# Kernel optimization log

Hardware: AMD Instinct MI355X
Metric: run time of the kernel (lower is better)

## Reference

```python
import jax, jax.numpy as jnp
import numpy as np

N_NODES = 100000
N_EDGES = 3200000
N_GRAPHS = 64
NODE_FEATS = 32
LATENT = [32, 32, 32, 1]
OUT_DIM = 128
TOTAL_LATENT = sum(LATENT)  # 97


def setup_inputs() -> dict:
    key = jax.random.key(0)
    ks = jax.random.split(key, 16)
    node_feat = jax.random.normal(ks[0], (N_NODES, NODE_FEATS), dtype=jnp.float32)
    src = jax.random.randint(ks[1], (N_EDGES,), 0, N_NODES)
    dst = jax.random.randint(ks[2], (N_EDGES,), 0, N_NODES)
    graph_ids = jnp.sort(jax.random.randint(ks[3], (N_NODES,), 0, N_GRAPHS))
    # layer weights: Linear(in, out) -> W [in, out], b [out]
    dims = [NODE_FEATS] + LATENT
    inp = {
        'node_feat': node_feat,
        'src': src,
        'dst': dst,
        'graph_ids': graph_ids,
        'num_graphs': N_GRAPHS,
    }
    for i in range(len(LATENT)):
        inp[f'W{i}'] = 0.1 * jax.random.normal(ks[4 + 2 * i], (dims[i], dims[i + 1]), dtype=jnp.float32)
        inp[f'b{i}'] = 0.1 * jax.random.normal(ks[5 + 2 * i], (dims[i + 1],), dtype=jnp.float32)
    inp['Wout'] = 0.1 * jax.random.normal(ks[12], (TOTAL_LATENT, OUT_DIM), dtype=jnp.float32)
    inp['bout'] = 0.1 * jax.random.normal(ks[13], (OUT_DIM,), dtype=jnp.float32)
    return inp


def reference(node_feat, W0, b0, W1, b1, W2, b2, W3, b3, Wout, bout,
              src, dst, graph_ids, num_graphs):
    N = node_feat.shape[0]
    # node_degs = deg + 1 (adjacency row sums + 1)
    degs = jax.ops.segment_sum(jnp.ones_like(dst, dtype=node_feat.dtype), dst, num_segments=N)
    node_degs = (degs + 1.0)[:, None]  # [N, 1]

    params = [(W0, b0), (W1, b1), (W2, b2), (W3, b3)]
    h = node_feat
    cats = []
    for W, b in params:
        # n2npool = A @ h + h  (sparse SpMM via edge-list segment sum)
        agg = jax.ops.segment_sum(h[src], dst, num_segments=N) + h
        h = jnp.tanh((agg @ W + b) / node_degs)
        cats.append(h)
    hcat = jnp.concatenate(cats, axis=1)  # [N, 97]

    # per-graph sum pooling
    pooled = jax.ops.segment_sum(hcat, graph_ids, num_segments=num_graphs)  # [G, 97]
    # relu(relu(linear)) == relu(linear)
    out = jax.nn.relu(pooled @ Wout + bout)
    return out
```

## Files before the change

kernel.cpp:

```cpp
#include <hip/hip_runtime.h>
#include <hip/hip_bf16.h>


#define NFEAT 32
#define TOTLAT 97
#define NGRAPH 64
#define OUTDIM 128
#define BSHIFT 9
#define NPB 512
#define MAXBUCK 256
#define CH 8192

__global__ __launch_bounds__(256) void hist_kernel(const int* __restrict__ dst,
                                                   int* __restrict__ bucket_cnt,
                                                   int E, int nbuck) {
    __shared__ int h[MAXBUCK];
    for (int i = threadIdx.x; i < nbuck; i += blockDim.x) h[i] = 0;
    __syncthreads();
    int e0 = blockIdx.x * CH, e1 = min(e0 + CH, E);
    const int4* d4 = (const int4*)dst;
    int k0 = e0 >> 2, nk = (e1 - e0) >> 2;
    for (int k = k0 + threadIdx.x; k < k0 + nk; k += blockDim.x) {
        int4 v = d4[k];
        atomicAdd(&h[v.x >> BSHIFT], 1);
        atomicAdd(&h[v.y >> BSHIFT], 1);
        atomicAdd(&h[v.z >> BSHIFT], 1);
        atomicAdd(&h[v.w >> BSHIFT], 1);
    }
    for (int e = e0 + (nk << 2) + threadIdx.x; e < e1; e += blockDim.x)
        atomicAdd(&h[dst[e] >> BSHIFT], 1);
    __syncthreads();
    for (int i = threadIdx.x; i < nbuck; i += blockDim.x)
        if (h[i]) atomicAdd(&bucket_cnt[i], h[i]);
}

__global__ void bucket_scan_kernel(const int* __restrict__ bucket_cnt,
                                   int* __restrict__ bucket_start,
                                   int* __restrict__ bucket_cursor,
                                   int* __restrict__ row_ptr,
                                   int N, int E, int nbuck) {
    __shared__ int s[MAXBUCK];
    int i = threadIdx.x;
    int v = (i < nbuck) ? bucket_cnt[i] : 0;
    s[i] = v;
    __syncthreads();
    for (int d = 1; d < MAXBUCK; d <<= 1) {
        int t = (i >= d) ? s[i - d] : 0;
        __syncthreads();
        if (i >= d) s[i] += t;
        __syncthreads();
    }
    if (i < nbuck) {
        int excl = s[i] - v;
        bucket_start[i] = excl;
        bucket_cursor[i] = excl;
    }
    if (i == 0) { bucket_start[nbuck] = E; row_ptr[N] = E; }
}

__global__ __launch_bounds__(256) void part_kernel(const int* __restrict__ src,
                                                   const int* __restrict__ dst,
                                                   int* __restrict__ bucket_cursor,
                                                   int2* __restrict__ pairs,
                                                   int E, int nbuck) {
    __shared__ int h[MAXBUCK];
    __shared__ int gb[MAXBUCK];
    for (int i = threadIdx.x; i < nbuck; i += blockDim.x) h[i] = 0;
    __syncthreads();
    int e0 = blockIdx.x * CH, e1 = min(e0 + CH, E);
    const int4* d4 = (const int4*)dst;
    const int4* s4 = (const int4*)src;
    int k0 = e0 >> 2, nk = (e1 - e0) >> 2;
    for (int k = k0 + threadIdx.x; k < k0 + nk; k += blockDim.x) {
        int4 v = d4[k];
        atomicAdd(&h[v.x >> BSHIFT], 1);
        atomicAdd(&h[v.y >> BSHIFT], 1);
        atomicAdd(&h[v.z >> BSHIFT], 1);
        atomicAdd(&h[v.w >> BSHIFT], 1);
    }
    for (int e = e0 + (nk << 2) + threadIdx.x; e < e1; e += blockDim.x)
        atomicAdd(&h[dst[e] >> BSHIFT], 1);
    __syncthreads();
    for (int i = threadIdx.x; i < nbuck; i += blockDim.x) {
        int c = h[i];
        gb[i] = c ? atomicAdd(&bucket_cursor[i], c) : 0;
        h[i] = 0;
    }
    __syncthreads();
    for (int k = k0 + threadIdx.x; k < k0 + nk; k += blockDim.x) {
        int4 d = d4[k];
        int4 s = s4[k];
        int b, r;
        b = d.x >> BSHIFT; r = atomicAdd(&h[b], 1); pairs[gb[b] + r] = make_int2(s.x, d.x);
        b = d.y >> BSHIFT; r = atomicAdd(&h[b], 1); pairs[gb[b] + r] = make_int2(s.y, d.y);
        b = d.z >> BSHIFT; r = atomicAdd(&h[b], 1); pairs[gb[b] + r] = make_int2(s.z, d.z);
        b = d.w >> BSHIFT; r = atomicAdd(&h[b], 1); pairs[gb[b] + r] = make_int2(s.w, d.w);
    }
    for (int e = e0 + (nk << 2) + threadIdx.x; e < e1; e += blockDim.x) {
        int dv = dst[e];
        int b = dv >> BSHIFT;
        int r = atomicAdd(&h[b], 1);
        pairs[gb[b] + r] = make_int2(src[e], dv);
    }
}

__global__ __launch_bounds__(NPB) void csr_kernel(const int2* __restrict__ pairs,
                                                  const int* __restrict__ bucket_start,
                                                  int* __restrict__ row_ptr,
                                                  int* __restrict__ col_idx,
                                                  float* __restrict__ inv_deg, int N) {
    __shared__ int deg[NPB];
    __shared__ int scn[NPB];
    int b = blockIdx.x;
    int n0 = b << BSHIFT;
    int tid = threadIdx.x;
    deg[tid] = 0;
    __syncthreads();
    int e0 = bucket_start[b], e1 = bucket_start[b + 1];
    for (int e = e0 + tid; e < e1; e += NPB) {
        int2 p = pairs[e];
        atomicAdd(&deg[p.y - n0], 1);
    }
    __syncthreads();
    int v = deg[tid];
    scn[tid] = v;
    __syncthreads();
    for (int d = 1; d < NPB; d <<= 1) {
        int t = (tid >= d) ? scn[tid - d] : 0;
        __syncthreads();
        if (tid >= d) scn[tid] += t;
        __syncthreads();
    }
    int excl = scn[tid] - v;
    int n = n0 + tid;
    if (n < N) {
        row_ptr[n] = e0 + excl;
        inv_deg[n] = 1.0f / ((float)v + 1.0f);
    }
    deg[tid] = excl;
    __syncthreads();
    for (int e = e0 + tid; e < e1; e += NPB) {
        int2 p = pairs[e];
        int r = atomicAdd(&deg[p.y - n0], 1);
        col_idx[e0 + r] = p.x;
    }
}

template <int OUT_COLS>
__global__ __launch_bounds__(256) void layer_kernel(
    const float* __restrict__ h_in, float* __restrict__ h_out,
    const float* __restrict__ W, const float* __restrict__ b,
    const int* __restrict__ row_ptr, const int* __restrict__ col_idx,
    const float* __restrict__ inv_deg, const int* __restrict__ graph_ids,
    float* __restrict__ pooled, int pool_col, int N)
{
    const int t = blockIdx.x * blockDim.x + threadIdx.x;
    int n = t >> 3;
    const int l8 = t & 7;
    const int f0 = l8 * 4;
    const int lane = threadIdx.x & 63;
    const bool valid = n < N;
    if (!valid) n = N - 1;

    const float4* __restrict__ h4 = (const float4*)h_in;

    int beg = row_ptr[n];
    int end = row_ptr[n + 1];
    int len = end - beg;
    float4 self = h4[(size_t)n * 8 + l8];
    float4 acc = self;

    for (int e = beg; e < end; e += 32) {
        int base = e + l8 * 4;
        int my0 = __builtin_nontemporal_load(&col_idx[base + 0]);
        int my1 = __builtin_nontemporal_load(&col_idx[base + 1]);
        int my2 = __builtin_nontemporal_load(&col_idx[base + 2]);
        int my3 = __builtin_nontemporal_load(&col_idx[base + 3]);
        int rem = end - e;
#pragma unroll
        for (int sl = 0; sl < 8; ++sl) {
            int i0 = __shfl(my0, sl, 8);
            int i1 = __shfl(my1, sl, 8);
            int i2 = __shfl(my2, sl, 8);
            int i3 = __shfl(my3, sl, 8);
            int j = sl * 4;
            i0 = (j + 0 < rem) ? i0 : n;
            i1 = (j + 1 < rem) ? i1 : n;
            i2 = (j + 2 < rem) ? i2 : n;
            i3 = (j + 3 < rem) ? i3 : n;
            float4 v0 = h4[(size_t)i0 * 8 + l8];
            float4 v1 = h4[(size_t)i1 * 8 + l8];
            float4 v2 = h4[(size_t)i2 * 8 + l8];
            float4 v3 = h4[(size_t)i3 * 8 + l8];
            acc.x += v0.x; acc.y += v0.y; acc.z += v0.z; acc.w += v0.w;
            acc.x += v1.x; acc.y += v1.y; acc.z += v1.z; acc.w += v1.w;
            acc.x += v2.x; acc.y += v2.y; acc.z += v2.z; acc.w += v2.w;
            acc.x += v3.x; acc.y += v3.y; acc.z += v3.z; acc.w += v3.w;
        }
    }
    float fk = (float)(((len + 31) & ~31) - len);
    acc.x -= fk * self.x; acc.y -= fk * self.y;
    acc.z -= fk * self.z; acc.w -= fk * self.w;

    float ideg = inv_deg[n];
    int g = graph_ids[n];
    int g0 = __builtin_amdgcn_readfirstlane(g);
    bool g_uniform = __all(g == g0);

    if (OUT_COLS == NFEAT) {
        float4 o = *(const float4*)&b[f0];
#pragma unroll
        for (int sl = 0; sl < 8; ++sl) {
            float a0 = __shfl(acc.x, sl, 8);
            float a1 = __shfl(acc.y, sl, 8);
            float a2 = __shfl(acc.z, sl, 8);
            float a3 = __shfl(acc.w, sl, 8);
            float4 w0 = *(const float4*)&W[(sl * 4 + 0) * NFEAT + f0];
            float4 w1 = *(const float4*)&W[(sl * 4 + 1) * NFEAT + f0];
            float4 w2 = *(const float4*)&W[(sl * 4 + 2) * NFEAT + f0];
            float4 w3 = *(const float4*)&W[(sl * 4 + 3) * NFEAT + f0];
            o.x += a0 * w0.x + a1 * w1.x + a2 * w2.x + a3 * w3.x;
            o.y += a0 * w0.y + a1 * w1.y + a2 * w2.y + a3 * w3.y;
            o.z += a0 * w0.z + a1 * w1.z + a2 * w2.z + a3 * w3.z;
            o.w += a0 * w0.w + a1 * w1.w + a2 * w2.w + a3 * w3.w;
        }
        float4 v;
        v.x = tanhf(o.x * ideg);
        v.y = tanhf(o.y * ideg);
        v.z = tanhf(o.z * ideg);
        v.w = tanhf(o.w * ideg);
        if (valid)
            *(float4*)&h_out[(size_t)n * NFEAT + f0] = v;

        float4 c;
        c.x = valid ? v.x : 0.0f;
        c.y = valid ? v.y : 0.0f;
        c.z = valid ? v.z : 0.0f;
        c.w = valid ? v.w : 0.0f;
        if (g_uniform) {
            c.x += __shfl_xor(c.x, 8);  c.x += __shfl_xor(c.x, 16);  c.x += __shfl_xor(c.x, 32);
            c.y += __shfl_xor(c.y, 8);  c.y += __shfl_xor(c.y, 16);  c.y += __shfl_xor(c.y, 32);
            c.z += __shfl_xor(c.z, 8);  c.z += __shfl_xor(c.z, 16);  c.z += __shfl_xor(c.z, 32);
            c.w += __shfl_xor(c.w, 8);  c.w += __shfl_xor(c.w, 16);  c.w += __shfl_xor(c.w, 32);
            if (lane < 8) {
                float* p = &pooled[g0 * TOTLAT + pool_col + f0];
                atomicAdd(p + 0, c.x);
                atomicAdd(p + 1, c.y);
                atomicAdd(p + 2, c.z);
                atomicAdd(p + 3, c.w);
            }
        } else if (valid) {
            float* p = &pooled[g * TOTLAT + pool_col + f0];
            atomicAdd(p + 0, v.x);
            atomicAdd(p + 1, v.y);
            atomicAdd(p + 2, v.z);
            atomicAdd(p + 3, v.w);
        }
    } else {
        float4 wv = *(const float4*)&W[f0];
        float p = acc.x * wv.x + acc.y * wv.y + acc.z * wv.z + acc.w * wv.w;
        p += __shfl_xor(p, 1);
        p += __shfl_xor(p, 2);
        p += __shfl_xor(p, 4);
        float v = tanhf((p + b[0]) * ideg);
        float c = (valid && l8 == 0) ? v : 0.0f;
        if (g_uniform) {
            c += __shfl_xor(c, 8); c += __shfl_xor(c, 16); c += __shfl_xor(c, 32);
            if (lane == 0)
                atomicAdd(&pooled[g0 * TOTLAT + pool_col], c);
        } else if (valid && l8 == 0) {
            atomicAdd(&pooled[g * TOTLAT + pool_col], v);
        }
    }
}

__global__ void final_kernel(const float* __restrict__ pooled, const float* __restrict__ Wout,
                             const float* __restrict__ bout, float* __restrict__ out) {
    int g = blockIdx.x;
    int o = threadIdx.x;
    float s = bout[o];
#pragma unroll 4
    for (int k = 0; k < TOTLAT; ++k)
        s += pooled[g * TOTLAT + k] * Wout[k * OUTDIM + o];
    out[g * OUTDIM + o] = fmaxf(s, 0.0f);
}

extern "C" void kernel_launch(void* const* d_in, const int* in_sizes, int n_in,
                              void* d_out, int out_size, void* d_ws, size_t ws_size,
                              hipStream_t stream) {
    const float* node_feat = (const float*)d_in[0];
    const int*   src       = (const int*)d_in[1];
    const int*   dst       = (const int*)d_in[2];
    const int*   graph_ids = (const int*)d_in[3];
    const float* W0 = (const float*)d_in[5];
    const float* b0 = (const float*)d_in[6];
    const float* W1 = (const float*)d_in[7];
    const float* b1 = (const float*)d_in[8];
    const float* W2 = (const float*)d_in[9];
    const float* b2 = (const float*)d_in[10];
    const float* W3 = (const float*)d_in[11];
    const float* b3 = (const float*)d_in[12];
    const float* Wout = (const float*)d_in[13];
    const float* bout = (const float*)d_in[14];
    float* out = (float*)d_out;

    const int N = in_sizes[0] / NFEAT;
    const int E = in_sizes[1];
    const int nbuck = (N + NPB - 1) >> BSHIFT;

    char* ws = (char*)d_ws;
    size_t off = 0;
    auto carve = [&](size_t bytes) -> void* {
        void* p = ws + off;
        off = (off + bytes + 255) & ~(size_t)255;
        return p;
    };
    int*   bucket_cnt    = (int*)carve((size_t)MAXBUCK * 4);
    int*   bucket_start  = (int*)carve((size_t)(MAXBUCK + 1) * 4);
    int*   bucket_cursor = (int*)carve((size_t)MAXBUCK * 4);
    int*   row_ptr       = (int*)carve((size_t)(N + 1) * 4);
    int*   col_idx       = (int*)carve((size_t)(E + 32) * 4);
    float* inv_deg       = (float*)carve((size_t)N * 4);
    float* hA            = (float*)carve((size_t)N * NFEAT * 4);
    float* hB            = (float*)carve((size_t)N * NFEAT * 4);
    float* pooled        = (float*)carve((size_t)NGRAPH * TOTLAT * 4);
    int2*  pairs         = (int2*)hA;

    hipMemsetAsync(bucket_cnt, 0, (size_t)MAXBUCK * 4, stream);
    hipMemsetAsync(pooled, 0, (size_t)NGRAPH * TOTLAT * 4, stream);

    const int nchunks = (E + CH - 1) / CH;
    hist_kernel<<<nchunks, 256, 0, stream>>>(dst, bucket_cnt, E, nbuck);
    bucket_scan_kernel<<<1, MAXBUCK, 0, stream>>>(bucket_cnt, bucket_start, bucket_cursor,
                                                  row_ptr, N, E, nbuck);
    part_kernel<<<nchunks, 256, 0, stream>>>(src, dst, bucket_cursor, pairs, E, nbuck);
    csr_kernel<<<nbuck, NPB, 0, stream>>>(pairs, bucket_start, row_ptr, col_idx, inv_deg, N);

    const int lblocks = (N * 8 + 255) / 256;
    layer_kernel<32><<<lblocks, 256, 0, stream>>>(node_feat, hA, W0, b0, row_ptr, col_idx,
                                                  inv_deg, graph_ids, pooled, 0, N);
    layer_kernel<32><<<lblocks, 256, 0, stream>>>(hA, hB, W1, b1, row_ptr, col_idx,
                                                  inv_deg, graph_ids, pooled, 32, N);
    layer_kernel<32><<<lblocks, 256, 0, stream>>>(hB, hA, W2, b2, row_ptr, col_idx,
                                                  inv_deg, graph_ids, pooled, 64, N);
    layer_kernel<1><<<lblocks, 256, 0, stream>>>(hA, nullptr, W3, b3, row_ptr, col_idx,
                                                 inv_deg, graph_ids, pooled, 96, N);

    final_kernel<<<NGRAPH, OUTDIM, 0, stream>>>(pooled, Wout, bout, out);
}
```

Baseline: 591.3 us.

## Reassociate last GNN layer to aggregate scalar projections and split agg/mlp kernels

The final layer's projection W3 is applied before neighbour aggregation, so the last sparse gather reads one float per edge instead of a 32-float row. Each layer is also split into a pure aggregation kernel and a separate dense MLP/tanh/pooling kernel, with the aggregation kernel given a higher occupancy hint. The aim is to cut gather bandwidth in the last layer and lighten register pressure in the gather loop. The cost is extra kernel launches and an extra round trip of the N×32 intermediate through memory per layer.

Measured after the change: 584.6 us. No clear change (-1.1%).

```diff
diff --git a/kernel.cpp b/kernel.cpp
--- a/kernel.cpp
+++ b/kernel.cpp
@@ -146,21 +146,14 @@
     }
 }
 
-template <int OUT_COLS>
-__global__ __launch_bounds__(256) void layer_kernel(
-    const float* __restrict__ h_in, float* __restrict__ h_out,
-    const float* __restrict__ W, const float* __restrict__ b,
-    const int* __restrict__ row_ptr, const int* __restrict__ col_idx,
-    const float* __restrict__ inv_deg, const int* __restrict__ graph_ids,
-    float* __restrict__ pooled, int pool_col, int N)
+__global__ __launch_bounds__(256, 8) void agg_kernel(
+    const float* __restrict__ h_in, float* __restrict__ agg,
+    const int* __restrict__ row_ptr, const int* __restrict__ col_idx, int N)
 {
     const int t = blockIdx.x * blockDim.x + threadIdx.x;
     int n = t >> 3;
     const int l8 = t & 7;
-    const int f0 = l8 * 4;
-    const int lane = threadIdx.x & 63;
-    const bool valid = n < N;
-    if (!valid) n = N - 1;
+    if (n >= N) return;
 
     const float4* __restrict__ h4 = (const float4*)h_in;
 
@@ -192,85 +185,141 @@
             float4 v1 = h4[(size_t)i1 * 8 + l8];
             float4 v2 = h4[(size_t)i2 * 8 + l8];
             float4 v3 = h4[(size_t)i3 * 8 + l8];
-            acc.x += v0.x; acc.y += v0.y; acc.z += v0.z; acc.w += v0.w;
-            acc.x += v1.x; acc.y += v1.y; acc.z += v1.z; acc.w += v1.w;
-            acc.x += v2.x; acc.y += v2.y; acc.z += v2.z; acc.w += v2.w;
-            acc.x += v3.x; acc.y += v3.y; acc.z += v3.z; acc.w += v3.w;
+            acc.x += v0.x + v1.x + v2.x + v3.x;
+            acc.y += v0.y + v1.y + v2.y + v3.y;
+            acc.z += v0.z + v1.z + v2.z + v3.z;
+            acc.w += v0.w + v1.w + v2.w + v3.w;
         }
     }
     float fk = (float)(((len + 31) & ~31) - len);
     acc.x -= fk * self.x; acc.y -= fk * self.y;
     acc.z -= fk * self.z; acc.w -= fk * self.w;
 
+    ((float4*)agg)[(size_t)n * 8 + l8] = acc;
+}
+
+template <bool EMIT_Y>
+__global__ __launch_bounds__(256) void mlp_kernel(
+    float* __restrict__ hbuf,
+    const float* __restrict__ W, const float* __restrict__ b,
+    const float* __restrict__ inv_deg, const int* __restrict__ graph_ids,
+    float* __restrict__ pooled, int pool_col,
+    const float* __restrict__ W3, float* __restrict__ y, int N)
+{
+    const int t = blockIdx.x * blockDim.x + threadIdx.x;
+    int n = t >> 3;
+    const int l8 = t & 7;
+    const int f0 = l8 * 4;
+    const int lane = threadIdx.x & 63;
+    const bool valid = n < N;
+    if (!valid) n = N - 1;
+
+    float4 acc = ((const float4*)hbuf)[(size_t)n * 8 + l8];
     float ideg = inv_deg[n];
     int g = graph_ids[n];
     int g0 = __builtin_amdgcn_readfirstlane(g);
     bool g_uniform = __all(g == g0);
 
-    if (OUT_COLS == NFEAT) {
-        float4 o = *(const float4*)&b[f0];
+    float4 o = *(const float4*)&b[f0];
 #pragma unroll
-        for (int sl = 0; sl < 8; ++sl) {
-            float a0 = __shfl(acc.x, sl, 8);
-            float a1 = __shfl(acc.y, sl, 8);
-            float a2 = __shfl(acc.z, sl, 8);
-            float a3 = __shfl(acc.w, sl, 8);
-            float4 w0 = *(const float4*)&W[(sl * 4 + 0) * NFEAT + f0];
-            float4 w1 = *(const float4*)&W[(sl * 4 + 1) * NFEAT + f0];
-            float4 w2 = *(const float4*)&W[(sl * 4 + 2) * NFEAT + f0];
-            float4 w3 = *(const float4*)&W[(sl * 4 + 3) * NFEAT + f0];
-            o.x += a0 * w0.x + a1 * w1.x + a2 * w2.x + a3 * w3.x;
-            o.y += a0 * w0.y + a1 * w1.y + a2 * w2.y + a3 * w3.y;
-            o.z += a0 * w0.z + a1 * w1.z + a2 * w2.z + a3 * w3.z;
-            o.w += a0 * w0.w + a1 * w1.w + a2 * w2.w + a3 * w3.w;
-        }
-        float4 v;
-        v.x = tanhf(o.x * ideg);
-        v.y = tanhf(o.y * ideg);
-        v.z = tanhf(o.z * ideg);
-        v.w = tanhf(o.w * ideg);
+    for (int sl = 0; sl < 8; ++sl) {
+        float a0 = __shfl(acc.x, sl, 8);
+        float a1 = __shfl(acc.y, sl, 8);
+        float a2 = __shfl(acc.z, sl, 8);
+        float a3 = __shfl(acc.w, sl, 8);
+        float4 w0 = *(const float4*)&W[(sl * 4 + 0) * NFEAT + f0];
+        float4 w1 = *(const float4*)&W[(sl * 4 + 1) * NFEAT + f0];
+        float4 w2 = *(const float4*)&W[(sl * 4 + 2) * NFEAT + f0];
+        float4 w3 = *(const float4*)&W[(sl * 4 + 3) * NFEAT + f0];
+        o.x += a0 * w0.x + a1 * w1.x + a2 * w2.x + a3 * w3.x;
+        o.y += a0 * w0.y + a1 * w1.y + a2 * w2.y + a3 * w3.y;
+        o.z += a0 * w0.z + a1 * w1.z + a2 * w2.z + a3 * w3.z;
+        o.w += a0 * w0.w + a1 * w1.w + a2 * w2.w + a3 * w3.w;
+    }
+    float4 v;
+    v.x = tanhf(o.x * ideg);
+    v.y = tanhf(o.y * ideg);
+    v.z = tanhf(o.z * ideg);
+    v.w = tanhf(o.w * ideg);
+
+    if (!EMIT_Y) {
         if (valid)
-            *(float4*)&h_out[(size_t)n * NFEAT + f0] = v;
-
-        float4 c;
-        c.x = valid ? v.x : 0.0f;
-        c.y = valid ? v.y : 0.0f;
-        c.z = valid ? v.z : 0.0f;
-        c.w = valid ? v.w : 0.0f;
-        if (g_uniform) {
-            c.x += __shfl_xor(c.x, 8);  c.x += __shfl_xor(c.x, 16);  c.x += __shfl_xor(c.x, 32);
-            c.y += __shfl_xor(c.y, 8);  c.y += __shfl_xor(c.y, 16);  c.y += __shfl_xor(c.y, 32);
-            c.z += __shfl_xor(c.z, 8);  c.z += __shfl_xor(c.z, 16);  c.z += __shfl_xor(c.z, 32);
-            c.w += __shfl_xor(c.w, 8);  c.w += __shfl_xor(c.w, 16);  c.w += __shfl_xor(c.w, 32);
-            if (lane < 8) {
-                float* p = &pooled[g0 * TOTLAT + pool_col + f0];
-                atomicAdd(p + 0, c.x);
-                atomicAdd(p + 1, c.y);
-                atomicAdd(p + 2, c.z);
-                atomicAdd(p + 3, c.w);
-            }
-        } else if (valid) {
-            float* p = &pooled[g * TOTLAT + pool_col + f0];
-            atomicAdd(p + 0, v.x);
-            atomicAdd(p + 1, v.y);
-            atomicAdd(p + 2, v.z);
-            atomicAdd(p + 3, v.w);
-        }
+            ((float4*)hbuf)[(size_t)n * 8 + l8] = v;
     } else {
-        float4 wv = *(const float4*)&W[f0];
-        float p = acc.x * wv.x + acc.y * wv.y + acc.z * wv.z + acc.w * wv.w;
+        float4 wv = *(const float4*)&W3[f0];
+        float p = v.x * wv.x + v.y * wv.y + v.z * wv.z + v.w * wv.w;
         p += __shfl_xor(p, 1);
         p += __shfl_xor(p, 2);
         p += __shfl_xor(p, 4);
-        float v = tanhf((p + b[0]) * ideg);
-        float c = (valid && l8 == 0) ? v : 0.0f;
-        if (g_uniform) {
-            c += __shfl_xor(c, 8); c += __shfl_xor(c, 16); c += __shfl_xor(c, 32);
-            if (lane == 0)
-                atomicAdd(&pooled[g0 * TOTLAT + pool_col], c);
-        } else if (valid && l8 == 0) {
-            atomicAdd(&pooled[g * TOTLAT + pool_col], v);
+        if (valid && l8 == 0) y[n] = p;
+    }
+
+    float4 c;
+    c.x = valid ? v.x : 0.0f;
+    c.y = valid ? v.y : 0.0f;
+    c.z = valid ? v.z : 0.0f;
+    c.w = valid ? v.w : 0.0f;
+    if (g_uniform) {
+        c.x += __shfl_xor(c.x, 8);  c.x += __shfl_xor(c.x, 16);  c.x += __shfl_xor(c.x, 32);
+        c.y += __shfl_xor(c.y, 8);  c.y += __shfl_xor(c.y, 16);  c.y += __shfl_xor(c.y, 32);
+        c.z += __shfl_xor(c.z, 8);  c.z += __shfl_xor(c.z, 16);  c.z += __shfl_xor(c.z, 32);
+        c.w += __shfl_xor(c.w, 8);  c.w += __shfl_xor(c.w, 16);  c.w += __shfl_xor(c.w, 32);
+        if (lane < 8) {
+            float* p = &pooled[g0 * TOTLAT + pool_col + f0];
+            atomicAdd(p + 0, c.x);
+            atomicAdd(p + 1, c.y);
+            atomicAdd(p + 2, c.z);
+            atomicAdd(p + 3, c.w);
         }
+    } else if (valid) {
+        float* p = &pooled[g * TOTLAT + pool_col + f0];
+        atomicAdd(p + 0, v.x);
+        atomicAdd(p + 1, v.y);
+        atomicAdd(p + 2, v.z);
+        atomicAdd(p + 3, v.w);
+    }
+}
+
+__global__ __launch_bounds__(256) void agg3_kernel(
+    const float* __restrict__ y, const float* __restrict__ b3,
+    const int* __restrict__ row_ptr, const int* __restrict__ col_idx,
+    const float* __restrict__ inv_deg, const int* __restrict__ graph_ids,
+    float* __restrict__ pooled, int N)
+{
+    int n = blockIdx.x * blockDim.x + threadIdx.x;
+    const bool valid = n < N;
+    if (!valid) n = N - 1;
+
+    int beg = row_ptr[n];
+    int end = row_ptr[n + 1];
+    float s = y[n];
+    int e = beg;
+    for (; e + 8 <= end; e += 8) {
+        float a0 = y[col_idx[e + 0]];
+        float a1 = y[col_idx[e + 1]];
+        float a2 = y[col_idx[e + 2]];
+        float a3 = y[col_idx[e + 3]];
+        float a4 = y[col_idx[e + 4]];
+        float a5 = y[col_idx[e + 5]];
+        float a6 = y[col_idx[e + 6]];
+        float a7 = y[col_idx[e + 7]];
+        s += ((a0 + a1) + (a2 + a3)) + ((a4 + a5) + (a6 + a7));
+    }
+    for (; e < end; ++e)
+        s += y[col_idx[e]];
+
+    float v = tanhf((s + b3[0]) * inv_deg[n]);
+
+    int g = graph_ids[n];
+    int g0 = __builtin_amdgcn_readfirstlane(g);
+    float c = valid ? v : 0.0f;
+    if (__all(g == g0)) {
+        c += __shfl_xor(c, 1);  c += __shfl_xor(c, 2);  c += __shfl_xor(c, 4);
+        c += __shfl_xor(c, 8);  c += __shfl_xor(c, 16); c += __shfl_xor(c, 32);
+        if ((threadIdx.x & 63) == 0)
+            atomicAdd(&pooled[g0 * TOTLAT + 96], c);
+    } else if (valid) {
+        atomicAdd(&pooled[g * TOTLAT + 96], v);
     }
 }
 
@@ -323,6 +372,7 @@
     float* inv_deg       = (float*)carve((size_t)N * 4);
     float* hA            = (float*)carve((size_t)N * NFEAT * 4);
     float* hB            = (float*)carve((size_t)N * NFEAT * 4);
+    float* y             = (float*)carve((size_t)N * 4);
     float* pooled        = (float*)carve((size_t)NGRAPH * TOTLAT * 4);
     int2*  pairs         = (int2*)hA;
 
@@ -337,14 +387,17 @@
     csr_kernel<<<nbuck, NPB, 0, stream>>>(pairs, bucket_start, row_ptr, col_idx, inv_deg, N);
 
     const int lblocks = (N * 8 + 255) / 256;
-    layer_kernel<32><<<lblocks, 256, 0, stream>>>(node_feat, hA, W0, b0, row_ptr, col_idx,
-                                                  inv_deg, graph_ids, pooled, 0, N);
-    layer_kernel<32><<<lblocks, 256, 0, stream>>>(hA, hB, W1, b1, row_ptr, col_idx,
-                                                  inv_deg, graph_ids, pooled, 32, N);
-    layer_kernel<32><<<lblocks, 256, 0, stream>>>(hB, hA, W2, b2, row_ptr, col_idx,
-                                                  inv_deg, graph_ids, pooled, 64, N);
-    layer_kernel<1><<<lblocks, 256, 0, stream>>>(hA, nullptr, W3, b3, row_ptr, col_idx,
-                                                 inv_deg, graph_ids, pooled, 96, N);
+    agg_kernel<<<lblocks, 256, 0, stream>>>(node_feat, hA, row_ptr, col_idx, N);
+    mlp_kernel<false><<<lblocks, 256, 0, stream>>>(hA, W0, b0, inv_deg, graph_ids,
+                                                   pooled, 0, nullptr, nullptr, N);
+    agg_kernel<<<lblocks, 256, 0, stream>>>(hA, hB, row_ptr, col_idx, N);
+    mlp_kernel<false><<<lblocks, 256, 0, stream>>>(hB, W1, b1, inv_deg, graph_ids,
+                                                   pooled, 32, nullptr, nullptr, N);
+    agg_kernel<<<lblocks, 256, 0, stream>>>(hB, hA, row_ptr, col_idx, N);
+    mlp_kernel<true><<<lblocks, 256, 0, stream>>>(hA, W2, b2, inv_deg, graph_ids,
+                                                  pooled, 64, W3, y, N);
+    agg3_kernel<<<(N + 255) / 256, 256, 0, stream>>>(y, b3, row_ptr, col_idx, inv_deg,
+                                                     graph_ids, pooled, N);
 
     final_kernel<<<NGRAPH, OUTDIM, 0, stream>>>(pooled, Wout, bout, out);
 }
```
